# Kernel tuning notes

Measured on AMD Instinct MI355X. Metric: run time of the kernel, lower is better.

The kernel has to match this reference:

```python
import jax, jax.numpy as jnp
import numpy as np

B, S, H, I = 2, 2048, 4096, 11008  # batch, seq, hidden_size, intermediate_size (Llama-7B)


def setup_inputs() -> dict:
    key = jax.random.key(0)
    ks = jax.random.split(key, 11)
    # int8 activations and weights (SmoothQuant W8A8)
    hidden_states = jax.random.randint(ks[0], (B, S, H), -128, 128, dtype=jnp.int8)
    w_gate = jax.random.randint(ks[1], (I, H), -128, 128, dtype=jnp.int8)
    w_up = jax.random.randint(ks[2], (I, H), -128, 128, dtype=jnp.int8)
    w_down = jax.random.randint(ks[3], (H, I), -128, 128, dtype=jnp.int8)
    # dequant scales (alpha = input_scale * weight_scale), small positive
    gate_a = jax.random.uniform(ks[4], (1,), dtype=jnp.float32) * 1e-4 + 1e-5
    up_a = jax.random.uniform(ks[5], (1,), dtype=jnp.float32) * 1e-4 + 1e-5
    down_a = jax.random.uniform(ks[6], (1,), dtype=jnp.float32) * 1e-4 + 1e-5
    # fp32 biases
    gate_b = jax.random.normal(ks[7], (I,), dtype=jnp.float32) * 0.01
    up_b = jax.random.normal(ks[8], (I,), dtype=jnp.float32) * 0.01
    down_b = jax.random.normal(ks[9], (H,), dtype=jnp.float32) * 0.01
    # requantization scale for down_proj input
    down_scale = jax.random.uniform(ks[10], (1,), dtype=jnp.float32) * 0.05 + 0.01
    return {
        "hidden_states": hidden_states,
        "w_gate": w_gate, "w_up": w_up, "w_down": w_down,
        "gate_a": gate_a, "gate_b": gate_b,
        "up_a": up_a, "up_b": up_b,
        "down_a": down_a, "down_b": down_b,
        "down_scale": down_scale,
    }


def _i8_gemm(x_i8, w_i8):
    return jnp.einsum("bsk,nk->bsn", x_i8, w_i8, preferred_element_type=jnp.int32)


def reference(hidden_states, w_gate, w_up, w_down,
              gate_a, gate_b, up_a, up_b, down_a, down_b, down_scale):
    # gate_proj: W8A8 GEMM -> dequant (alpha) + fp32 bias -> fused SiLU
    g = _i8_gemm(hidden_states, w_gate).astype(jnp.float32) * gate_a[0] + gate_b
    gate_out = g * jax.nn.sigmoid(g)  # SiLU
    # up_proj: W8A8 GEMM -> dequant + fp32 bias
    up_out = _i8_gemm(hidden_states, w_up).astype(jnp.float32) * up_a[0] + up_b
    inter = gate_out * up_out
    # requantize to int8 for down_proj input
    q = jnp.clip(jnp.round(inter / down_scale[0]), -128, 127).astype(jnp.int8)
    # down_proj: W8A8 GEMM -> dequant + fp32 bias
    down_out = _i8_gemm(q, w_down).astype(jnp.float32) * down_a[0] + down_b
    return down_out  # [B, S, H] fp32
```

## Files before the change

### kernel.cpp

```cpp
#include <hip/hip_runtime.h>
#include <cstdint>


typedef int v4i  __attribute__((ext_vector_type(4)));
typedef int v16i __attribute__((ext_vector_type(16)));

typedef const void __attribute__((address_space(1)))* gas_ptr;
typedef void __attribute__((address_space(3)))* las_ptr;

static constexpr int M_TOT = 4096;
static constexpr int HDIM  = 4096;
static constexpr int IDIM  = 11008;

#define MFMA_I8(a, b, c) __builtin_amdgcn_mfma_i32_32x32x32_i8((a), (b), (c), 0, 0, 0)
#define BAR()      asm volatile("s_barrier" ::: "memory")
#define WAIT_VM0() asm volatile("s_waitcnt vmcnt(0)" ::: "memory")
#define SETPRIO(P) __builtin_amdgcn_s_setprio(P)

__device__ __forceinline__ void gload16(const int8_t* g, int8_t* l) {
  __builtin_amdgcn_global_load_lds((gas_ptr)g, (las_ptr)l, 16, 0, 0);
}

__device__ __forceinline__ v4i frag128(const int8_t* lds, int row, int c) {
  const int pair = row >> 1;
  const int slot = ((c << 1) | (row & 1)) ^ (pair & 15);
  return *(const v4i*)(lds + pair * 256 + slot * 16);
}

__device__ __forceinline__ void relmap128(int rel, int& row, int& col) {
  const int pair = rel >> 4;
  const int sl = (rel & 15) ^ (pair & 15);
  row = 2 * pair + (sl & 1);
  col = (sl >> 1) * 16;
}

__device__ __forceinline__ void pack16(const int* __restrict__ src,
                                       int8_t* __restrict__ dst, int t) {
  const int4* s = (const int4*)(src) + t * 4;
  int4 v0 = s[0], v1 = s[1], v2 = s[2], v3 = s[3];
  int p0 = (v0.x & 0xff) | ((v0.y & 0xff) << 8) | ((v0.z & 0xff) << 16) | (v0.w << 24);
  int p1 = (v1.x & 0xff) | ((v1.y & 0xff) << 8) | ((v1.z & 0xff) << 16) | (v1.w << 24);
  int p2 = (v2.x & 0xff) | ((v2.y & 0xff) << 8) | ((v2.z & 0xff) << 16) | (v2.w << 24);
  int p3 = (v3.x & 0xff) | ((v3.y & 0xff) << 8) | ((v3.z & 0xff) << 16) | (v3.w << 24);
  ((int4*)dst)[t] = make_int4(p0, p1, p2, p3);
}

static constexpr int CX = (M_TOT * HDIM) / 16;
static constexpr int CW = (IDIM * HDIM) / 16;
static constexpr int CTOT = CX + 3 * CW;

__global__ __launch_bounds__(256) void k_pack_all(
    const int* __restrict__ X32, const int* __restrict__ Wg32,
    const int* __restrict__ Wu32, const int* __restrict__ Wd32,
    int8_t* __restrict__ Xp, int8_t* __restrict__ Wgp,
    int8_t* __restrict__ Wup, int8_t* __restrict__ Wdp) {
  int t = blockIdx.x * blockDim.x + threadIdx.x;
  if (t >= CTOT) return;
  if (t < CX)               { pack16(X32,  Xp,  t); return; }
  t -= CX;
  if (t < CW)               { pack16(Wg32, Wgp, t); return; }
  t -= CW;
  if (t < CW)               { pack16(Wu32, Wup, t); return; }
  t -= CW;
  pack16(Wd32, Wdp, t);
}

__global__ __launch_bounds__(512, 2) void k_gateup(
    const int8_t* __restrict__ X,
    const int8_t* __restrict__ Wg,
    const int8_t* __restrict__ Wu,
    const float* __restrict__ gate_a, const float* __restrict__ gate_b,
    const float* __restrict__ up_a,   const float* __restrict__ up_b,
    const float* __restrict__ down_scale,
    int8_t* __restrict__ Q) {
  __shared__ __align__(16) int8_t lds8[2 * 65536];

  const int tid  = threadIdx.x;
  const int lane = tid & 63;
  const int wave = tid >> 6;
  const int wm   = wave >> 2;
  const int wn   = wave & 3;
  const int half = lane >> 5;
  const int ln31 = lane & 31;

  const int m0 = blockIdx.x * 256;
  const int n0 = blockIdx.y * 128;

  const int8_t* Ab = X  + (size_t)m0 * HDIM;
  const int8_t* Gb = Wg + (size_t)n0 * HDIM;
  const int8_t* Ub = Wu + (size_t)n0 * HDIM;

  int r0, c0, r1, c1, r2, c2, r3, c3;
  relmap128(tid,        r0, c0);
  relmap128(tid + 512,  r1, c1);
  relmap128(tid + 1024, r2, c2);
  relmap128(tid + 1536, r3, c3);
  const size_t oA0 = (size_t)r0 * HDIM + c0;
  const size_t oA1 = (size_t)r1 * HDIM + c1;
  const size_t oA2 = (size_t)r2 * HDIM + c2;
  const size_t oA3 = (size_t)r3 * HDIM + c3;

  v16i accG[4], accU[4];
#pragma unroll
  for (int i = 0; i < 4; ++i)
#pragma unroll
    for (int e = 0; e < 16; ++e) { accG[i][e] = 0; accU[i][e] = 0; }

  const int rA = wm * 128 + ln31;
  const int rB = wn * 32 + ln31;

  {
    int8_t* sb = lds8;
    gload16(Ab + oA0, sb + tid * 16);
    gload16(Ab + oA1, sb + (tid + 512) * 16);
    gload16(Ab + oA2, sb + (tid + 1024) * 16);
    gload16(Ab + oA3, sb + (tid + 1536) * 16);
    gload16(Gb + oA0, sb + 32768 + tid * 16);
    gload16(Gb + oA1, sb + 32768 + (tid + 512) * 16);
    gload16(Ub + oA0, sb + 49152 + tid * 16);
    gload16(Ub + oA1, sb + 49152 + (tid + 512) * 16);
    WAIT_VM0();
    BAR();
  }

  const int NT = HDIM / 128;
  for (int s = 0; s < NT; ++s) {
    const int8_t* bufA = lds8 + (s & 1) * 65536;
    const int8_t* bufG = bufA + 32768;
    const int8_t* bufU = bufA + 49152;

    if (s + 1 < NT) {
      int8_t* sb = lds8 + ((s + 1) & 1) * 65536;
      const int8_t* ap = Ab + (size_t)(s + 1) * 128;
      const int8_t* gp = Gb + (size_t)(s + 1) * 128;
      const int8_t* up = Ub + (size_t)(s + 1) * 128;
      gload16(ap + oA0, sb + tid * 16);
      gload16(ap + oA1, sb + (tid + 512) * 16);
      gload16(ap + oA2, sb + (tid + 1024) * 16);
      gload16(ap + oA3, sb + (tid + 1536) * 16);
      gload16(gp + oA0, sb + 32768 + tid * 16);
      gload16(gp + oA1, sb + 32768 + (tid + 512) * 16);
      gload16(up + oA0, sb + 49152 + tid * 16);
      gload16(up + oA1, sb + 49152 + (tid + 512) * 16);
    }

    SETPRIO(1);
#pragma unroll
    for (int ks = 0; ks < 4; ++ks) {
      const int c = 2 * ks + half;
      v4i a0 = frag128(bufA, rA,      c);
      v4i a1 = frag128(bufA, rA + 32, c);
      v4i a2 = frag128(bufA, rA + 64, c);
      v4i a3 = frag128(bufA, rA + 96, c);
      v4i gg = frag128(bufG, rB, c);
      v4i uu = frag128(bufU, rB, c);
      accG[0] = MFMA_I8(a0, gg, accG[0]);
      accU[0] = MFMA_I8(a0, uu, accU[0]);
      accG[1] = MFMA_I8(a1, gg, accG[1]);
      accU[1] = MFMA_I8(a1, uu, accU[1]);
      accG[2] = MFMA_I8(a2, gg, accG[2]);
      accU[2] = MFMA_I8(a2, uu, accU[2]);
      accG[3] = MFMA_I8(a3, gg, accG[3]);
      accU[3] = MFMA_I8(a3, uu, accU[3]);
    }
    SETPRIO(0);

    if (s + 1 < NT) {
      WAIT_VM0();
      BAR();
    }
  }

  const float ga = gate_a[0];
  const float ua = up_a[0];
  const float inv_ds = 1.0f / down_scale[0];
  const int n = n0 + wn * 32 + ln31;
  const float gb = gate_b[n];
  const float ub = up_b[n];

#pragma unroll
  for (int tm = 0; tm < 4; ++tm) {
#pragma unroll
    for (int r = 0; r < 16; ++r) {
      const int row_l = (r & 3) + 8 * (r >> 2) + 4 * half;
      const int m = m0 + wm * 128 + tm * 32 + row_l;
      const float g = (float)accG[tm][r] * ga + gb;
      const float u = (float)accU[tm][r] * ua + ub;
      const float sg = g / (1.0f + __expf(-g));
      const float inter = sg * u;
      float qf = rintf(inter * inv_ds);
      qf = fminf(127.0f, fmaxf(-128.0f, qf));
      Q[(size_t)m * IDIM + n] = (int8_t)qf;
    }
  }
}

__global__ __launch_bounds__(512, 2) void k_down(
    const int8_t* __restrict__ Qm,
    const int8_t* __restrict__ Wd,
    const float* __restrict__ down_a, const float* __restrict__ down_b,
    float* __restrict__ Out) {
  __shared__ __align__(16) int8_t lds8[2 * 65536];

  const int tid  = threadIdx.x;
  const int lane = tid & 63;
  const int wave = tid >> 6;
  const int wm   = wave >> 2;
  const int wn   = wave & 3;
  const int half = lane >> 5;
  const int ln31 = lane & 31;

  const int m0 = blockIdx.x * 256;
  const int n0 = blockIdx.y * 256;

  const int8_t* Ab = Qm + (size_t)m0 * IDIM;
  const int8_t* Bb = Wd + (size_t)n0 * IDIM;

  int r0, c0, r1, c1, r2, c2, r3, c3;
  relmap128(tid,        r0, c0);
  relmap128(tid + 512,  r1, c1);
  relmap128(tid + 1024, r2, c2);
  relmap128(tid + 1536, r3, c3);
  const size_t o0 = (size_t)r0 * IDIM + c0;
  const size_t o1 = (size_t)r1 * IDIM + c1;
  const size_t o2 = (size_t)r2 * IDIM + c2;
  const size_t o3 = (size_t)r3 * IDIM + c3;

  v16i acc[4][2];
#pragma unroll
  for (int i = 0; i < 4; ++i)
#pragma unroll
    for (int j = 0; j < 2; ++j)
#pragma unroll
      for (int e = 0; e < 16; ++e) acc[i][j][e] = 0;

  const int rA = wm * 128 + ln31;
  const int rB = wn * 64 + ln31;

  {
    int8_t* sb = lds8;
    gload16(Ab + o0, sb + tid * 16);
    gload16(Ab + o1, sb + (tid + 512) * 16);
    gload16(Ab + o2, sb + (tid + 1024) * 16);
    gload16(Ab + o3, sb + (tid + 1536) * 16);
    gload16(Bb + o0, sb + 32768 + tid * 16);
    gload16(Bb + o1, sb + 32768 + (tid + 512) * 16);
    gload16(Bb + o2, sb + 32768 + (tid + 1024) * 16);
    gload16(Bb + o3, sb + 32768 + (tid + 1536) * 16);
    WAIT_VM0();
    BAR();
  }

  const int NT = IDIM / 128;
  for (int s = 0; s < NT; ++s) {
    const int8_t* bufA = lds8 + (s & 1) * 65536;
    const int8_t* bufB = bufA + 32768;

    if (s + 1 < NT) {
      int8_t* sb = lds8 + ((s + 1) & 1) * 65536;
      const int8_t* ap = Ab + (size_t)(s + 1) * 128;
      const int8_t* bp = Bb + (size_t)(s + 1) * 128;
      gload16(ap + o0, sb + tid * 16);
      gload16(ap + o1, sb + (tid + 512) * 16);
      gload16(ap + o2, sb + (tid + 1024) * 16);
      gload16(ap + o3, sb + (tid + 1536) * 16);
      gload16(bp + o0, sb + 32768 + tid * 16);
      gload16(bp + o1, sb + 32768 + (tid + 512) * 16);
      gload16(bp + o2, sb + 32768 + (tid + 1024) * 16);
      gload16(bp + o3, sb + 32768 + (tid + 1536) * 16);
    }

    SETPRIO(1);
#pragma unroll
    for (int ks = 0; ks < 4; ++ks) {
      const int c = 2 * ks + half;
      v4i a0 = frag128(bufA, rA,      c);
      v4i a1 = frag128(bufA, rA + 32, c);
      v4i a2 = frag128(bufA, rA + 64, c);
      v4i a3 = frag128(bufA, rA + 96, c);
      v4i b0 = frag128(bufB, rB,      c);
      v4i b1 = frag128(bufB, rB + 32, c);
      acc[0][0] = MFMA_I8(a0, b0, acc[0][0]);
      acc[0][1] = MFMA_I8(a0, b1, acc[0][1]);
      acc[1][0] = MFMA_I8(a1, b0, acc[1][0]);
      acc[1][1] = MFMA_I8(a1, b1, acc[1][1]);
      acc[2][0] = MFMA_I8(a2, b0, acc[2][0]);
      acc[2][1] = MFMA_I8(a2, b1, acc[2][1]);
      acc[3][0] = MFMA_I8(a3, b0, acc[3][0]);
      acc[3][1] = MFMA_I8(a3, b1, acc[3][1]);
    }
    SETPRIO(0);

    if (s + 1 < NT) {
      WAIT_VM0();
      BAR();
    }
  }

  const float da = down_a[0];
#pragma unroll
  for (int tn = 0; tn < 2; ++tn) {
    const int n = n0 + wn * 64 + tn * 32 + ln31;
    const float db = down_b[n];
#pragma unroll
    for (int tm = 0; tm < 4; ++tm) {
#pragma unroll
      for (int r = 0; r < 16; ++r) {
        const int row_l = (r & 3) + 8 * (r >> 2) + 4 * half;
        const int m = m0 + wm * 128 + tm * 32 + row_l;
        Out[(size_t)m * HDIM + n] = (float)acc[tm][tn][r] * da + db;
      }
    }
  }
}

extern "C" void kernel_launch(void* const* d_in, const int* in_sizes, int n_in,
                              void* d_out, int out_size, void* d_ws, size_t ws_size,
                              hipStream_t stream) {
  const int* X32        = (const int*)d_in[0];
  const int* Wg32       = (const int*)d_in[1];
  const int* Wu32       = (const int*)d_in[2];
  const int* Wd32       = (const int*)d_in[3];
  const float* gate_a   = (const float*)d_in[4];
  const float* gate_b   = (const float*)d_in[5];
  const float* up_a     = (const float*)d_in[6];
  const float* up_b     = (const float*)d_in[7];
  const float* down_a   = (const float*)d_in[8];
  const float* down_b   = (const float*)d_in[9];
  const float* down_scale = (const float*)d_in[10];
  float* Out = (float*)d_out;

  const size_t nX = (size_t)M_TOT * HDIM;
  const size_t nW = (size_t)IDIM * HDIM;

  int8_t* Q   = (int8_t*)d_ws;
  int8_t* Xp  = Q   + nW;
  int8_t* Wgp = Xp  + nX;
  int8_t* Wup = Wgp + nW;
  int8_t* Wdp = Wup + nW;

  k_pack_all<<<(CTOT + 255) / 256, 256, 0, stream>>>(X32, Wg32, Wu32, Wd32,
                                                     Xp, Wgp, Wup, Wdp);

  k_gateup<<<dim3(M_TOT / 256, IDIM / 128), dim3(512), 0, stream>>>(
      Xp, Wgp, Wup, gate_a, gate_b, up_a, up_b, down_scale, Q);

  k_down<<<dim3(M_TOT / 256, HDIM / 256), dim3(512), 0, stream>>>(
      Q, Wdp, down_a, down_b, Out);
}
```

Measured before the change: 1.092 ms.

## Switch int8 GEMMs to 16x16x64 MFMA with row-wise XOR-swizzled LDS layout

```diff
diff --git a/kernel.cpp b/kernel.cpp
--- a/kernel.cpp
+++ b/kernel.cpp
@@ -3,7 +3,6 @@
 
 
 typedef int v4i  __attribute__((ext_vector_type(4)));
-typedef int v16i __attribute__((ext_vector_type(16)));
 
 typedef const void __attribute__((address_space(1)))* gas_ptr;
 typedef void __attribute__((address_space(3)))* las_ptr;
@@ -12,26 +11,24 @@
 static constexpr int HDIM  = 4096;
 static constexpr int IDIM  = 11008;
 
-#define MFMA_I8(a, b, c) __builtin_amdgcn_mfma_i32_32x32x32_i8((a), (b), (c), 0, 0, 0)
-#define BAR()      asm volatile("s_barrier" ::: "memory")
-#define WAIT_VM0() asm volatile("s_waitcnt vmcnt(0)" ::: "memory")
-#define SETPRIO(P) __builtin_amdgcn_s_setprio(P)
+#define MFMA16(a, b, c) __builtin_amdgcn_mfma_i32_16x16x64_i8((a), (b), (c), 0, 0, 0)
+#define BAR()        asm volatile("s_barrier" ::: "memory")
+#define WAIT_VM0()   asm volatile("s_waitcnt vmcnt(0)" ::: "memory")
+#define SETPRIO(P)   __builtin_amdgcn_s_setprio(P)
 
 __device__ __forceinline__ void gload16(const int8_t* g, int8_t* l) {
   __builtin_amdgcn_global_load_lds((gas_ptr)g, (las_ptr)l, 16, 0, 0);
 }
 
-__device__ __forceinline__ v4i frag128(const int8_t* lds, int row, int c) {
-  const int pair = row >> 1;
-  const int slot = ((c << 1) | (row & 1)) ^ (pair & 15);
-  return *(const v4i*)(lds + pair * 256 + slot * 16);
-}
-
-__device__ __forceinline__ void relmap128(int rel, int& row, int& col) {
-  const int pair = rel >> 4;
-  const int sl = (rel & 15) ^ (pair & 15);
-  row = 2 * pair + (sl & 1);
-  col = (sl >> 1) * 16;
+__device__ __forceinline__ v4i fragR(const int8_t* region, int row, int cb) {
+  const int slot = cb ^ (row & 7);
+  return *(const v4i*)(region + row * 128 + slot * 16);
+}
+
+__device__ __forceinline__ size_t srcmap(int q, int ld) {
+  const int r = q >> 3;
+  const int c = (q & 7) ^ (r & 7);
+  return (size_t)r * ld + c * 16;
 }
 
 __device__ __forceinline__ void pack16(const int* __restrict__ src,
@@ -80,8 +77,8 @@
   const int wave = tid >> 6;
   const int wm   = wave >> 2;
   const int wn   = wave & 3;
-  const int half = lane >> 5;
-  const int ln31 = lane & 31;
+  const int r16  = lane & 15;
+  const int quad = lane >> 4;
 
   const int m0 = blockIdx.x * 256;
   const int n0 = blockIdx.y * 128;
@@ -90,107 +87,99 @@
   const int8_t* Gb = Wg + (size_t)n0 * HDIM;
   const int8_t* Ub = Wu + (size_t)n0 * HDIM;
 
-  int r0, c0, r1, c1, r2, c2, r3, c3;
-  relmap128(tid,        r0, c0);
-  relmap128(tid + 512,  r1, c1);
-  relmap128(tid + 1024, r2, c2);
-  relmap128(tid + 1536, r3, c3);
-  const size_t oA0 = (size_t)r0 * HDIM + c0;
-  const size_t oA1 = (size_t)r1 * HDIM + c1;
-  const size_t oA2 = (size_t)r2 * HDIM + c2;
-  const size_t oA3 = (size_t)r3 * HDIM + c3;
-
-  v16i accG[4], accU[4];
-#pragma unroll
-  for (int i = 0; i < 4; ++i)
-#pragma unroll
-    for (int e = 0; e < 16; ++e) { accG[i][e] = 0; accU[i][e] = 0; }
-
-  const int rA = wm * 128 + ln31;
-  const int rB = wn * 32 + ln31;
-
-  {
-    int8_t* sb = lds8;
-    gload16(Ab + oA0, sb + tid * 16);
-    gload16(Ab + oA1, sb + (tid + 512) * 16);
-    gload16(Ab + oA2, sb + (tid + 1024) * 16);
-    gload16(Ab + oA3, sb + (tid + 1536) * 16);
-    gload16(Gb + oA0, sb + 32768 + tid * 16);
-    gload16(Gb + oA1, sb + 32768 + (tid + 512) * 16);
-    gload16(Ub + oA0, sb + 49152 + tid * 16);
-    gload16(Ub + oA1, sb + 49152 + (tid + 512) * 16);
-    WAIT_VM0();
-    BAR();
+  size_t oA[4], oW[2];
+#pragma unroll
+  for (int j = 0; j < 4; ++j) oA[j] = srcmap(tid + j * 512, HDIM);
+#pragma unroll
+  for (int j = 0; j < 2; ++j) oW[j] = srcmap(tid + j * 512, HDIM);
+
+  v4i accG[8][2], accU[8][2];
+#pragma unroll
+  for (int i = 0; i < 8; ++i)
+#pragma unroll
+    for (int j = 0; j < 2; ++j)
+#pragma unroll
+      for (int e = 0; e < 4; ++e) { accG[i][j][e] = 0; accU[i][j][e] = 0; }
+
+#define GU_STAGE(t_, sb)                                                \
+  {                                                                     \
+    const size_t ks = (size_t)(t_) * 128;                               \
+    _Pragma("unroll")                                                   \
+    for (int j = 0; j < 4; ++j)                                         \
+      gload16(Ab + ks + oA[j], (sb) + (tid + j * 512) * 16);            \
+    _Pragma("unroll")                                                   \
+    for (int j = 0; j < 2; ++j) {                                       \
+      gload16(Gb + ks + oW[j], (sb) + 32768 + (tid + j * 512) * 16);    \
+      gload16(Ub + ks + oW[j], (sb) + 49152 + (tid + j * 512) * 16);    \
+    }                                                                   \
   }
 
   const int NT = HDIM / 128;
-  for (int s = 0; s < NT; ++s) {
-    const int8_t* bufA = lds8 + (s & 1) * 65536;
+
+  GU_STAGE(0, lds8)
+  WAIT_VM0();
+  BAR();
+
+  for (int t = 0; t < NT; ++t) {
+    const int8_t* bufA = lds8 + (t & 1) * 65536;
     const int8_t* bufG = bufA + 32768;
     const int8_t* bufU = bufA + 49152;
 
-    if (s + 1 < NT) {
-      int8_t* sb = lds8 + ((s + 1) & 1) * 65536;
-      const int8_t* ap = Ab + (size_t)(s + 1) * 128;
-      const int8_t* gp = Gb + (size_t)(s + 1) * 128;
-      const int8_t* up = Ub + (size_t)(s + 1) * 128;
-      gload16(ap + oA0, sb + tid * 16);
-      gload16(ap + oA1, sb + (tid + 512) * 16);
-      gload16(ap + oA2, sb + (tid + 1024) * 16);
-      gload16(ap + oA3, sb + (tid + 1536) * 16);
-      gload16(gp + oA0, sb + 32768 + tid * 16);
-      gload16(gp + oA1, sb + 32768 + (tid + 512) * 16);
-      gload16(up + oA0, sb + 49152 + tid * 16);
-      gload16(up + oA1, sb + 49152 + (tid + 512) * 16);
-    }
+    if (t + 1 < NT) GU_STAGE(t + 1, lds8 + ((t + 1) & 1) * 65536)
 
     SETPRIO(1);
 #pragma unroll
-    for (int ks = 0; ks < 4; ++ks) {
-      const int c = 2 * ks + half;
-      v4i a0 = frag128(bufA, rA,      c);
-      v4i a1 = frag128(bufA, rA + 32, c);
-      v4i a2 = frag128(bufA, rA + 64, c);
-      v4i a3 = frag128(bufA, rA + 96, c);
-      v4i gg = frag128(bufG, rB, c);
-      v4i uu = frag128(bufU, rB, c);
-      accG[0] = MFMA_I8(a0, gg, accG[0]);
-      accU[0] = MFMA_I8(a0, uu, accU[0]);
-      accG[1] = MFMA_I8(a1, gg, accG[1]);
-      accU[1] = MFMA_I8(a1, uu, accU[1]);
-      accG[2] = MFMA_I8(a2, gg, accG[2]);
-      accU[2] = MFMA_I8(a2, uu, accU[2]);
-      accG[3] = MFMA_I8(a3, gg, accG[3]);
-      accU[3] = MFMA_I8(a3, uu, accU[3]);
+    for (int kh = 0; kh < 2; ++kh) {
+      const int cb = kh * 4 + quad;
+      v4i a_[8], g_[2], u_[2];
+#pragma unroll
+      for (int mi = 0; mi < 8; ++mi)
+        a_[mi] = fragR(bufA, wm * 128 + mi * 16 + r16, cb);
+#pragma unroll
+      for (int ni = 0; ni < 2; ++ni) {
+        g_[ni] = fragR(bufG, wn * 32 + ni * 16 + r16, cb);
+        u_[ni] = fragR(bufU, wn * 32 + ni * 16 + r16, cb);
+      }
+#pragma unroll
+      for (int mi = 0; mi < 8; ++mi)
+#pragma unroll
+        for (int ni = 0; ni < 2; ++ni) {
+          accG[mi][ni] = MFMA16(a_[mi], g_[ni], accG[mi][ni]);
+          accU[mi][ni] = MFMA16(a_[mi], u_[ni], accU[mi][ni]);
+        }
     }
     SETPRIO(0);
 
-    if (s + 1 < NT) {
+    if (t + 1 < NT) {
       WAIT_VM0();
       BAR();
     }
   }
+#undef GU_STAGE
 
   const float ga = gate_a[0];
   const float ua = up_a[0];
   const float inv_ds = 1.0f / down_scale[0];
-  const int n = n0 + wn * 32 + ln31;
-  const float gb = gate_b[n];
-  const float ub = up_b[n];
-
-#pragma unroll
-  for (int tm = 0; tm < 4; ++tm) {
-#pragma unroll
-    for (int r = 0; r < 16; ++r) {
-      const int row_l = (r & 3) + 8 * (r >> 2) + 4 * half;
-      const int m = m0 + wm * 128 + tm * 32 + row_l;
-      const float g = (float)accG[tm][r] * ga + gb;
-      const float u = (float)accU[tm][r] * ua + ub;
-      const float sg = g / (1.0f + __expf(-g));
-      const float inter = sg * u;
-      float qf = rintf(inter * inv_ds);
-      qf = fminf(127.0f, fmaxf(-128.0f, qf));
-      Q[(size_t)m * IDIM + n] = (int8_t)qf;
+
+#pragma unroll
+  for (int ni = 0; ni < 2; ++ni) {
+    const int n = n0 + wn * 32 + ni * 16 + r16;
+    const float gb = gate_b[n];
+    const float ub = up_b[n];
+#pragma unroll
+    for (int mi = 0; mi < 8; ++mi) {
+      const int mbase = m0 + wm * 128 + mi * 16 + quad * 4;
+#pragma unroll
+      for (int e = 0; e < 4; ++e) {
+        const int m = mbase + e;
+        const float g = (float)accG[mi][ni][e] * ga + gb;
+        const float u = (float)accU[mi][ni][e] * ua + ub;
+        const float sg = g / (1.0f + __expf(-g));
+        const float inter = sg * u;
+        float qf = rintf(inter * inv_ds);
+        qf = fminf(127.0f, fmaxf(-128.0f, qf));
+        Q[(size_t)m * IDIM + n] = (int8_t)qf;
+      }
     }
   }
 }
@@ -207,8 +196,8 @@
   const int wave = tid >> 6;
   const int wm   = wave >> 2;
   const int wn   = wave & 3;
-  const int half = lane >> 5;
-  const int ln31 = lane & 31;
+  const int r16  = lane & 15;
+  const int quad = lane >> 4;
 
   const int m0 = blockIdx.x * 256;
   const int n0 = blockIdx.y * 256;
@@ -216,99 +205,81 @@
   const int8_t* Ab = Qm + (size_t)m0 * IDIM;
   const int8_t* Bb = Wd + (size_t)n0 * IDIM;
 
-  int r0, c0, r1, c1, r2, c2, r3, c3;
-  relmap128(tid,        r0, c0);
-  relmap128(tid + 512,  r1, c1);
-  relmap128(tid + 1024, r2, c2);
-  relmap128(tid + 1536, r3, c3);
-  const size_t o0 = (size_t)r0 * IDIM + c0;
-  const size_t o1 = (size_t)r1 * IDIM + c1;
-  const size_t o2 = (size_t)r2 * IDIM + c2;
-  const size_t o3 = (size_t)r3 * IDIM + c3;
-
-  v16i acc[4][2];
-#pragma unroll
-  for (int i = 0; i < 4; ++i)
-#pragma unroll
-    for (int j = 0; j < 2; ++j)
-#pragma unroll
-      for (int e = 0; e < 16; ++e) acc[i][j][e] = 0;
-
-  const int rA = wm * 128 + ln31;
-  const int rB = wn * 64 + ln31;
-
-  {
-    int8_t* sb = lds8;
-    gload16(Ab + o0, sb + tid * 16);
-    gload16(Ab + o1, sb + (tid + 512) * 16);
-    gload16(Ab + o2, sb + (tid + 1024) * 16);
-    gload16(Ab + o3, sb + (tid + 1536) * 16);
-    gload16(Bb + o0, sb + 32768 + tid * 16);
-    gload16(Bb + o1, sb + 32768 + (tid + 512) * 16);
-    gload16(Bb + o2, sb + 32768 + (tid + 1024) * 16);
-    gload16(Bb + o3, sb + 32768 + (tid + 1536) * 16);
-    WAIT_VM0();
-    BAR();
+  size_t oA[4], oB[4];
+#pragma unroll
+  for (int j = 0; j < 4; ++j) {
+    oA[j] = srcmap(tid + j * 512, IDIM);
+    oB[j] = oA[j];
+  }
+
+  v4i acc[8][4];
+#pragma unroll
+  for (int i = 0; i < 8; ++i)
+#pragma unroll
+    for (int j = 0; j < 4; ++j)
+#pragma unroll
+      for (int e = 0; e < 4; ++e) acc[i][j][e] = 0;
+
+#define DN_STAGE(t_, sb)                                                \
+  {                                                                     \
+    const size_t ks = (size_t)(t_) * 128;                               \
+    _Pragma("unroll")                                                   \
+    for (int j = 0; j < 4; ++j) {                                       \
+      gload16(Ab + ks + oA[j], (sb) + (tid + j * 512) * 16);            \
+      gload16(Bb + ks + oB[j], (sb) + 32768 + (tid + j * 512) * 16);    \
+    }                                                                   \
   }
 
   const int NT = IDIM / 128;
-  for (int s = 0; s < NT; ++s) {
-    const int8_t* bufA = lds8 + (s & 1) * 65536;
+
+  DN_STAGE(0, lds8)
+  WAIT_VM0();
+  BAR();
+
+  for (int t = 0; t < NT; ++t) {
+    const int8_t* bufA = lds8 + (t & 1) * 65536;
     const int8_t* bufB = bufA + 32768;
 
-    if (s + 1 < NT) {
-      int8_t* sb = lds8 + ((s + 1) & 1) * 65536;
-      const int8_t* ap = Ab + (size_t)(s + 1) * 128;
-      const int8_t* bp = Bb + (size_t)(s + 1) * 128;
-      gload16(ap + o0, sb + tid * 16);
-      gload16(ap + o1, sb + (tid + 512) * 16);
-      gload16(ap + o2, sb + (tid + 1024) * 16);
-      gload16(ap + o3, sb + (tid + 1536) * 16);
-      gload16(bp + o0, sb + 32768 + tid * 16);
-      gload16(bp + o1, sb + 32768 + (tid + 512) * 16);
-      gload16(bp + o2, sb + 32768 + (tid + 1024) * 16);
-      gload16(bp + o3, sb + 32768 + (tid + 1536) * 16);
-    }
+    if (t + 1 < NT) DN_STAGE(t + 1, lds8 + ((t + 1) & 1) * 65536)
 
     SETPRIO(1);
 #pragma unroll
-    for (int ks = 0; ks < 4; ++ks) {
-      const int c = 2 * ks + half;
-      v4i a0 = frag128(bufA, rA,      c);
-      v4i a1 = frag128(bufA, rA + 32, c);
-      v4i a2 = frag128(bufA, rA + 64, c);
-      v4i a3 = frag128(bufA, rA + 96, c);
-      v4i b0 = frag128(bufB, rB,      c);
-      v4i b1 = frag128(bufB, rB + 32, c);
-      acc[0][0] = MFMA_I8(a0, b0, acc[0][0]);
-      acc[0][1] = MFMA_I8(a0, b1, acc[0][1]);
-      acc[1][0] = MFMA_I8(a1, b0, acc[1][0]);
-      acc[1][1] = MFMA_I8(a1, b1, acc[1][1]);
-      acc[2][0] = MFMA_I8(a2, b0, acc[2][0]);
-      acc[2][1] = MFMA_I8(a2, b1, acc[2][1]);
-      acc[3][0] = MFMA_I8(a3, b0, acc[3][0]);
-      acc[3][1] = MFMA_I8(a3, b1, acc[3][1]);
+    for (int kh = 0; kh < 2; ++kh) {
+      const int cb = kh * 4 + quad;
+      v4i a_[8], b_[4];
+#pragma unroll
+      for (int mi = 0; mi < 8; ++mi)
+        a_[mi] = fragR(bufA, wm * 128 + mi * 16 + r16, cb);
+#pragma unroll
+      for (int ni = 0; ni < 4; ++ni)
+        b_[ni] = fragR(bufB, wn * 64 + ni * 16 + r16, cb);
+#pragma unroll
+      for (int mi = 0; mi < 8; ++mi)
+#pragma unroll
+        for (int ni = 0; ni < 4; ++ni)
+          acc[mi][ni] = MFMA16(a_[mi], b_[ni], acc[mi][ni]);
     }
     SETPRIO(0);
 
-    if (s + 1 < NT) {
+    if (t + 1 < NT) {
       WAIT_VM0();
       BAR();
     }
   }
+#undef DN_STAGE
 
   const float da = down_a[0];
 #pragma unroll
-  for (int tn = 0; tn < 2; ++tn) {
-    const int n = n0 + wn * 64 + tn * 32 + ln31;
+  for (int ni = 0; ni < 4; ++ni) {
+    const int n = n0 + wn * 64 + ni * 16 + r16;
     const float db = down_b[n];
 #pragma unroll
-    for (int tm = 0; tm < 4; ++tm) {
-#pragma unroll
-      for (int r = 0; r < 16; ++r) {
-        const int row_l = (r & 3) + 8 * (r >> 2) + 4 * half;
-        const int m = m0 + wm * 128 + tm * 32 + row_l;
-        Out[(size_t)m * HDIM + n] = (float)acc[tm][tn][r] * da + db;
+    for (int mi = 0; mi < 8; ++mi) {
+      const int mbase = m0 + wm * 128 + mi * 16 + quad * 4;
+#pragma unroll
+      for (int e = 0; e < 4; ++e) {
+        const int m = mbase + e;
+        Out[(size_t)m * HDIM + n] = (float)acc[mi][ni][e] * da + db;
       }
     }
   }
```

Result: faster. 1.041 ms (-4.6%).
